# Optimization experiments

Hardware: AMD Instinct MI355X
Metric: run time of the kernel (lower is better)

## Reference

```python
import jax, jax.numpy as jnp
import numpy as np

N = 100000
E = 625000
IN_C, HID_C, OUT_C = 128, 128, 128


def setup_inputs() -> dict:
    key = jax.random.key(0)
    ks = jax.random.split(key, 8)
    x = jax.random.normal(ks[0], (N, IN_C), dtype=jnp.float32)
    edge_index = jax.random.randint(ks[1], (2, E), 0, N, dtype=jnp.int64)
    # SAGEConv layer 1: lin_l (on aggregated neighbors, with bias), lin_r (on root, no bias)
    s1 = 1.0 / np.sqrt(IN_C)
    W1l = jax.random.uniform(ks[2], (HID_C, IN_C), minval=-s1, maxval=s1, dtype=jnp.float32)
    b1l = jax.random.uniform(ks[3], (HID_C,), minval=-s1, maxval=s1, dtype=jnp.float32)
    W1r = jax.random.uniform(ks[4], (HID_C, IN_C), minval=-s1, maxval=s1, dtype=jnp.float32)
    s2 = 1.0 / np.sqrt(HID_C)
    W2l = jax.random.uniform(ks[5], (OUT_C, HID_C), minval=-s2, maxval=s2, dtype=jnp.float32)
    b2l = jax.random.uniform(ks[6], (OUT_C,), minval=-s2, maxval=s2, dtype=jnp.float32)
    W2r = jax.random.uniform(ks[7], (OUT_C, HID_C), minval=-s2, maxval=s2, dtype=jnp.float32)
    return {"x": x, "edge_index": edge_index,
            "W1l": W1l, "b1l": b1l, "W1r": W1r,
            "W2l": W2l, "b2l": b2l, "W2r": W2r}


def _sage_conv(x, src, dst, Wl, bl, Wr, num_nodes):
    # mean aggregation of source features into destination nodes
    agg = jax.ops.segment_sum(x[src], dst, num_segments=num_nodes)  # [N, d]
    cnt = jax.ops.segment_sum(jnp.ones((src.shape[0],), dtype=x.dtype), dst,
                              num_segments=num_nodes)  # [N]
    mean = agg / jnp.maximum(cnt, 1.0)[:, None]  # zero-degree nodes stay 0
    return mean @ Wl.T + bl + x @ Wr.T


def reference(x, edge_index, W1l, b1l, W1r, W2l, b2l, W2r):
    src, dst = edge_index[0], edge_index[1]
    h = jax.nn.sigmoid(_sage_conv(x, src, dst, W1l, b1l, W1r, N))
    out = _sage_conv(h, src, dst, W2l, b2l, W2r, N)
    return out
```

## Files before the change

kernel.cpp:

```cpp
#include <hip/hip_runtime.h>
#include <math.h>

#define NN 100000
#define NE 625000
#define CC 128
#define CAP 32
#define NT2 1563
#define LSTR 264

typedef __attribute__((ext_vector_type(8))) short bf16x8;
typedef __attribute__((ext_vector_type(4))) float f32x4;

__device__ __forceinline__ unsigned short f2b(float f) {
    unsigned int u = __float_as_uint(f);
    unsigned int r = (u + 0x7FFFu + ((u >> 16) & 1u)) >> 16;
    return (unsigned short)r;
}
__device__ __forceinline__ float b2f(unsigned int h) {
    return __uint_as_float(h << 16);
}


__global__ void build_kernel(const int* __restrict__ src, const int* __restrict__ dst,
                             int* __restrict__ cnt, int* __restrict__ col) {
    int e = blockIdx.x * blockDim.x + threadIdx.x;
    if (e < NE) {
        int d = dst[e];
        int p = atomicAdd(&cnt[d], 1);
        if (p < CAP) col[d * CAP + p] = src[e];
    }
}


__global__ __launch_bounds__(256) void cvtX_kernel(const float* __restrict__ x,
                                                   unsigned short* __restrict__ xb) {
    size_t i = ((size_t)blockIdx.x * 256 + threadIdx.x) * 4;
    float4 v = *(const float4*)&x[i];
    ushort2 lo = { f2b(v.x), f2b(v.y) };
    ushort2 hi = { f2b(v.z), f2b(v.w) };
    *(ushort2*)&xb[i]     = lo;
    *(ushort2*)&xb[i + 2] = hi;
}


__global__ void cvtW_kernel(const float* __restrict__ W1l, const float* __restrict__ W1r,
                            const float* __restrict__ W2l, const float* __restrict__ W2r,
                            unsigned short* __restrict__ Wcat1,
                            unsigned short* __restrict__ Wcat2) {
    int i = blockIdx.x * blockDim.x + threadIdx.x;
    int layer = i >> 15;
    int local = i & 32767;
    int c = local >> 8;
    int k = local & 255;
    const float* Wl = layer ? W2l : W1l;
    const float* Wr = layer ? W2r : W1r;
    float v = (k < CC) ? Wl[c * CC + k] : Wr[c * CC + (k - CC)];
    (layer ? Wcat2 : Wcat1)[local] = f2b(v);
}


#define ACC8(u, m) \
    s0 = fmaf(m, b2f((u).x & 0xFFFFu), s0); s1 = fmaf(m, b2f((u).x >> 16), s1); \
    s2 = fmaf(m, b2f((u).y & 0xFFFFu), s2); s3 = fmaf(m, b2f((u).y >> 16), s3); \
    s4 = fmaf(m, b2f((u).z & 0xFFFFu), s4); s5 = fmaf(m, b2f((u).z >> 16), s5); \
    s6 = fmaf(m, b2f((u).w & 0xFFFFu), s6); s7 = fmaf(m, b2f((u).w >> 16), s7);

__global__ __launch_bounds__(256) void gather_kernel(const unsigned short* __restrict__ feat,
                                                     const int* __restrict__ cnt,
                                                     const int* __restrict__ col,
                                                     unsigned short* __restrict__ aggb) {
    int gtid = blockIdx.x * blockDim.x + threadIdx.x;
    int node = gtid >> 4;
    if (node >= NN) return;
    int c8 = (gtid & 15) * 8;
    int deg = cnt[node];
    int dmin = deg < CAP ? deg : CAP;
    const int* __restrict__ bucket = col + node * CAP;
    float s0 = 0, s1 = 0, s2 = 0, s3 = 0, s4 = 0, s5 = 0, s6 = 0, s7 = 0;
    int dpad = (dmin + 3) & ~3;
    for (int j = 0; j < dpad; j += 4) {
        int i1 = j + 1, i2 = j + 2, i3 = j + 3;
        float m1 = i1 < dmin ? 1.0f : 0.0f;
        float m2 = i2 < dmin ? 1.0f : 0.0f;
        float m3 = i3 < dmin ? 1.0f : 0.0f;
        if (i1 >= dmin) i1 = dmin - 1;
        if (i2 >= dmin) i2 = dmin - 1;
        if (i3 >= dmin) i3 = dmin - 1;
        int n0 = bucket[j], n1 = bucket[i1], n2 = bucket[i2], n3 = bucket[i3];
        uint4 u0 = *(const uint4*)&feat[(size_t)n0 * CC + c8];
        uint4 u1 = *(const uint4*)&feat[(size_t)n1 * CC + c8];
        uint4 u2 = *(const uint4*)&feat[(size_t)n2 * CC + c8];
        uint4 u3 = *(const uint4*)&feat[(size_t)n3 * CC + c8];
        ACC8(u0, 1.0f);
        ACC8(u1, m1);
        ACC8(u2, m2);
        ACC8(u3, m3);
    }
    float iv = 1.0f / (float)(deg > 0 ? deg : 1);
    uint4 o;
    o.x = (unsigned int)f2b(s0 * iv) | ((unsigned int)f2b(s1 * iv) << 16);
    o.y = (unsigned int)f2b(s2 * iv) | ((unsigned int)f2b(s3 * iv) << 16);
    o.z = (unsigned int)f2b(s4 * iv) | ((unsigned int)f2b(s5 * iv) << 16);
    o.w = (unsigned int)f2b(s6 * iv) | ((unsigned int)f2b(s7 * iv) << 16);
    *(uint4*)&aggb[(size_t)node * CC + c8] = o;
}


template<bool SIGMOID, bool OUT_FP32>
__global__ __launch_bounds__(256, 3) void gemm3_kernel(
        const unsigned short* __restrict__ aggb,
        const unsigned short* __restrict__ featb,
        const unsigned short* __restrict__ Wcat,
        const float* __restrict__ bias,
        void* __restrict__ outv) {
    __shared__ unsigned short Acat[64 * LSTR];

    const int t    = threadIdx.x;
    const int w    = t >> 6;
    const int lane = t & 63;
    const int m    = lane & 15;
    const int kq   = lane >> 4;
    const int col0 = w * 32;

    bf16x8 breg[2][8];
#pragma unroll
    for (int ct = 0; ct < 2; ++ct)
#pragma unroll
        for (int ks = 0; ks < 8; ++ks)
            breg[ct][ks] = *(const bf16x8*)(Wcat + (size_t)(col0 + ct * 16 + m) * 256 + ks * 32 + kq * 8);

    const float bias0 = bias[col0 + m];
    const float bias1 = bias[col0 + 16 + m];

    const int sr  = t >> 2;
    const int seg = t & 3;

    for (int rt = blockIdx.x; rt < NT2; rt += gridDim.x) {
        const int row0 = rt * 64;

        int gr = row0 + sr; if (gr >= NN) gr = NN - 1;
        const unsigned short* srcp = (seg < 2)
            ? (aggb  + (size_t)gr * CC + seg * 64)
            : (featb + (size_t)gr * CC + (seg - 2) * 64);
        bf16x8 st[8];
#pragma unroll
        for (int j = 0; j < 8; ++j) st[j] = *(const bf16x8*)(srcp + j * 8);

        __syncthreads();

        unsigned short* q = &Acat[sr * LSTR + seg * 64];
#pragma unroll
        for (int j = 0; j < 8; ++j) *(bf16x8*)(q + j * 8) = st[j];

        __syncthreads();

        f32x4 acc[4][2];
#pragma unroll
        for (int rt4 = 0; rt4 < 4; ++rt4)
#pragma unroll
            for (int ct = 0; ct < 2; ++ct) acc[rt4][ct] = (f32x4)0.0f;

#pragma unroll
        for (int ks = 0; ks < 8; ++ks) {
            bf16x8 a[4];
#pragma unroll
            for (int rt4 = 0; rt4 < 4; ++rt4)
                a[rt4] = *(const bf16x8*)&Acat[(rt4 * 16 + m) * LSTR + ks * 32 + kq * 8];
#pragma unroll
            for (int rt4 = 0; rt4 < 4; ++rt4) {
                acc[rt4][0] = __builtin_amdgcn_mfma_f32_16x16x32_bf16(a[rt4], breg[0][ks], acc[rt4][0], 0, 0, 0);
                acc[rt4][1] = __builtin_amdgcn_mfma_f32_16x16x32_bf16(a[rt4], breg[1][ks], acc[rt4][1], 0, 0, 0);
            }
        }

#pragma unroll
        for (int rt4 = 0; rt4 < 4; ++rt4) {
#pragma unroll
            for (int ct = 0; ct < 2; ++ct) {
                const int c = col0 + ct * 16 + m;
                const float bv = ct ? bias1 : bias0;
#pragma unroll
                for (int i = 0; i < 4; ++i) {
                    const int r = row0 + rt4 * 16 + kq * 4 + i;
                    if (r < NN) {
                        float v = acc[rt4][ct][i] + bv;
                        if (SIGMOID) v = 1.0f / (1.0f + __expf(-v));
                        if (OUT_FP32) ((float*)outv)[(size_t)r * CC + c] = v;
                        else ((unsigned short*)outv)[(size_t)r * CC + c] = f2b(v);
                    }
                }
            }
        }
    }
}


extern "C" void kernel_launch(void* const* d_in, const int* in_sizes, int n_in,
                              void* d_out, int out_size, void* d_ws, size_t ws_size,
                              hipStream_t stream) {
    const float* x   = (const float*)d_in[0];
    const int*   ei  = (const int*)d_in[1];
    const float* W1l = (const float*)d_in[2];
    const float* b1l = (const float*)d_in[3];
    const float* W1r = (const float*)d_in[4];
    const float* W2l = (const float*)d_in[5];
    const float* b2l = (const float*)d_in[6];
    const float* W2r = (const float*)d_in[7];
    float* out = (float*)d_out;

    const int* src = ei;
    const int* dst = ei + NE;

    int* cnt = (int*)d_ws;
    int* col = cnt + NN;
    unsigned short* Wcat1 = (unsigned short*)(col + NN * CAP);
    unsigned short* Wcat2 = Wcat1 + 128 * 256;
    unsigned short* xb    = Wcat2 + 128 * 256;
    unsigned short* aggb  = xb + (size_t)NN * CC;
    unsigned short* hb    = aggb + (size_t)NN * CC;

    hipMemsetAsync(cnt, 0, (size_t)NN * sizeof(int), stream);

    build_kernel<<<(NE + 255) / 256, 256, 0, stream>>>(src, dst, cnt, col);
    cvtX_kernel<<<(NN * CC / 4) / 256, 256, 0, stream>>>(x, xb);
    cvtW_kernel<<<256, 256, 0, stream>>>(W1l, W1r, W2l, W2r, Wcat1, Wcat2);

    const int GB = 782;

    gather_kernel<<<(NN * 16) / 256, 256, 0, stream>>>(xb, cnt, col, aggb);
    gemm3_kernel<true, false><<<GB, 256, 0, stream>>>(aggb, xb, Wcat1, b1l, hb);

    gather_kernel<<<(NN * 16) / 256, 256, 0, stream>>>(hb, cnt, col, aggb);
    gemm3_kernel<false, true><<<GB, 256, 0, stream>>>(aggb, hb, Wcat2, b2l, out);
}
```

Measured before the change: 252.5 us.

## Fuse neighbor mean-aggregation gather into the MFMA GEMM kernel

Removes the separate gather kernels and the intermediate bf16 aggregate buffer. Each GEMM block now gathers and averages neighbor features for its 64 rows directly into shared memory, then runs the same MFMA GEMM. This saves the global write and re-read of the aggregate and two kernel launches. In exchange, the GEMM kernel now carries latency-bound gathers with less parallelism per node (16 threads handle 4 nodes serially), and its occupancy hint drops from 3 to 2 blocks per CU.

```diff
diff --git a/kernel.cpp b/kernel.cpp
--- a/kernel.cpp
+++ b/kernel.cpp
@@ -65,51 +65,11 @@
     s4 = fmaf(m, b2f((u).z & 0xFFFFu), s4); s5 = fmaf(m, b2f((u).z >> 16), s5); \
     s6 = fmaf(m, b2f((u).w & 0xFFFFu), s6); s7 = fmaf(m, b2f((u).w >> 16), s7);
 
-__global__ __launch_bounds__(256) void gather_kernel(const unsigned short* __restrict__ feat,
-                                                     const int* __restrict__ cnt,
-                                                     const int* __restrict__ col,
-                                                     unsigned short* __restrict__ aggb) {
-    int gtid = blockIdx.x * blockDim.x + threadIdx.x;
-    int node = gtid >> 4;
-    if (node >= NN) return;
-    int c8 = (gtid & 15) * 8;
-    int deg = cnt[node];
-    int dmin = deg < CAP ? deg : CAP;
-    const int* __restrict__ bucket = col + node * CAP;
-    float s0 = 0, s1 = 0, s2 = 0, s3 = 0, s4 = 0, s5 = 0, s6 = 0, s7 = 0;
-    int dpad = (dmin + 3) & ~3;
-    for (int j = 0; j < dpad; j += 4) {
-        int i1 = j + 1, i2 = j + 2, i3 = j + 3;
-        float m1 = i1 < dmin ? 1.0f : 0.0f;
-        float m2 = i2 < dmin ? 1.0f : 0.0f;
-        float m3 = i3 < dmin ? 1.0f : 0.0f;
-        if (i1 >= dmin) i1 = dmin - 1;
-        if (i2 >= dmin) i2 = dmin - 1;
-        if (i3 >= dmin) i3 = dmin - 1;
-        int n0 = bucket[j], n1 = bucket[i1], n2 = bucket[i2], n3 = bucket[i3];
-        uint4 u0 = *(const uint4*)&feat[(size_t)n0 * CC + c8];
-        uint4 u1 = *(const uint4*)&feat[(size_t)n1 * CC + c8];
-        uint4 u2 = *(const uint4*)&feat[(size_t)n2 * CC + c8];
-        uint4 u3 = *(const uint4*)&feat[(size_t)n3 * CC + c8];
-        ACC8(u0, 1.0f);
-        ACC8(u1, m1);
-        ACC8(u2, m2);
-        ACC8(u3, m3);
-    }
-    float iv = 1.0f / (float)(deg > 0 ? deg : 1);
-    uint4 o;
-    o.x = (unsigned int)f2b(s0 * iv) | ((unsigned int)f2b(s1 * iv) << 16);
-    o.y = (unsigned int)f2b(s2 * iv) | ((unsigned int)f2b(s3 * iv) << 16);
-    o.z = (unsigned int)f2b(s4 * iv) | ((unsigned int)f2b(s5 * iv) << 16);
-    o.w = (unsigned int)f2b(s6 * iv) | ((unsigned int)f2b(s7 * iv) << 16);
-    *(uint4*)&aggb[(size_t)node * CC + c8] = o;
-}
-
-
 template<bool SIGMOID, bool OUT_FP32>
-__global__ __launch_bounds__(256, 3) void gemm3_kernel(
-        const unsigned short* __restrict__ aggb,
+__global__ __launch_bounds__(256, 2) void fgemm_kernel(
         const unsigned short* __restrict__ featb,
+        const int* __restrict__ cnt,
+        const int* __restrict__ colb,
         const unsigned short* __restrict__ Wcat,
         const float* __restrict__ bias,
         void* __restrict__ outv) {
@@ -132,25 +92,63 @@
     const float bias0 = bias[col0 + m];
     const float bias1 = bias[col0 + 16 + m];
 
-    const int sr  = t >> 2;
-    const int seg = t & 3;
+    const int l16 = t & 15;
+    const int g   = t >> 4;
+    const int c8  = l16 * 8;
 
     for (int rt = blockIdx.x; rt < NT2; rt += gridDim.x) {
         const int row0 = rt * 64;
 
-        int gr = row0 + sr; if (gr >= NN) gr = NN - 1;
-        const unsigned short* srcp = (seg < 2)
-            ? (aggb  + (size_t)gr * CC + seg * 64)
-            : (featb + (size_t)gr * CC + (seg - 2) * 64);
-        bf16x8 st[8];
-#pragma unroll
-        for (int j = 0; j < 8; ++j) st[j] = *(const bf16x8*)(srcp + j * 8);
+        bf16x8 st[4];
+#pragma unroll
+        for (int j = 0; j < 4; ++j) {
+            int fr = row0 + g + j * 16;
+            if (fr >= NN) fr = NN - 1;
+            st[j] = *(const bf16x8*)(featb + (size_t)fr * CC + c8);
+        }
+
+        uint4 aggv[4];
+#pragma unroll
+        for (int rr = 0; rr < 4; ++rr) {
+            const int node = row0 + g * 4 + rr;
+            int deg = (node < NN) ? cnt[node] : 0;
+            int dmin = deg < CAP ? deg : CAP;
+            const int* __restrict__ bucket = colb + (size_t)node * CAP;
+            float s0 = 0, s1 = 0, s2 = 0, s3 = 0, s4 = 0, s5 = 0, s6 = 0, s7 = 0;
+            int dpad = (dmin + 3) & ~3;
+            for (int j = 0; j < dpad; j += 4) {
+                int i1 = j + 1, i2 = j + 2, i3 = j + 3;
+                float m1 = i1 < dmin ? 1.0f : 0.0f;
+                float m2 = i2 < dmin ? 1.0f : 0.0f;
+                float m3 = i3 < dmin ? 1.0f : 0.0f;
+                if (i1 >= dmin) i1 = dmin - 1;
+                if (i2 >= dmin) i2 = dmin - 1;
+                if (i3 >= dmin) i3 = dmin - 1;
+                int n0 = bucket[j], n1 = bucket[i1], n2 = bucket[i2], n3 = bucket[i3];
+                uint4 u0 = *(const uint4*)&featb[(size_t)n0 * CC + c8];
+                uint4 u1 = *(const uint4*)&featb[(size_t)n1 * CC + c8];
+                uint4 u2 = *(const uint4*)&featb[(size_t)n2 * CC + c8];
+                uint4 u3 = *(const uint4*)&featb[(size_t)n3 * CC + c8];
+                ACC8(u0, 1.0f);
+                ACC8(u1, m1);
+                ACC8(u2, m2);
+                ACC8(u3, m3);
+            }
+            float iv = 1.0f / (float)(deg > 0 ? deg : 1);
+            aggv[rr].x = (unsigned int)f2b(s0 * iv) | ((unsigned int)f2b(s1 * iv) << 16);
+            aggv[rr].y = (unsigned int)f2b(s2 * iv) | ((unsigned int)f2b(s3 * iv) << 16);
+            aggv[rr].z = (unsigned int)f2b(s4 * iv) | ((unsigned int)f2b(s5 * iv) << 16);
+            aggv[rr].w = (unsigned int)f2b(s6 * iv) | ((unsigned int)f2b(s7 * iv) << 16);
+        }
 
         __syncthreads();
 
-        unsigned short* q = &Acat[sr * LSTR + seg * 64];
-#pragma unroll
-        for (int j = 0; j < 8; ++j) *(bf16x8*)(q + j * 8) = st[j];
+#pragma unroll
+        for (int rr = 0; rr < 4; ++rr)
+            *(uint4*)&Acat[(size_t)(g * 4 + rr) * LSTR + c8] = aggv[rr];
+#pragma unroll
+        for (int j = 0; j < 4; ++j)
+            *(bf16x8*)&Acat[(size_t)(g + j * 16) * LSTR + 128 + c8] = st[j];
 
         __syncthreads();
 
@@ -216,8 +214,7 @@
     unsigned short* Wcat1 = (unsigned short*)(col + NN * CAP);
     unsigned short* Wcat2 = Wcat1 + 128 * 256;
     unsigned short* xb    = Wcat2 + 128 * 256;
-    unsigned short* aggb  = xb + (size_t)NN * CC;
-    unsigned short* hb    = aggb + (size_t)NN * CC;
+    unsigned short* hb    = xb + (size_t)NN * CC;
 
     hipMemsetAsync(cnt, 0, (size_t)NN * sizeof(int), stream);
 
@@ -227,9 +224,6 @@
 
     const int GB = 782;
 
-    gather_kernel<<<(NN * 16) / 256, 256, 0, stream>>>(xb, cnt, col, aggb);
-    gemm3_kernel<true, false><<<GB, 256, 0, stream>>>(aggb, xb, Wcat1, b1l, hb);
-
-    gather_kernel<<<(NN * 16) / 256, 256, 0, stream>>>(hb, cnt, col, aggb);
-    gemm3_kernel<false, true><<<GB, 256, 0, stream>>>(aggb, hb, Wcat2, b2l, out);
-}
+    fgemm_kernel<true, false><<<GB, 256, 0, stream>>>(xb, cnt, col, Wcat1, b1l, hb);
+    fgemm_kernel<false, true><<<GB, 256, 0, stream>>>(hb, cnt, col, Wcat2, b2l, out);
+}
```

Result: slower. 269.5 us (+6.7%).
